# Kernel tuning notes

Hardware: AMD Instinct MI355X
Metric: run time of the kernel (lower is better)

The kernel has to match this reference:

```python
import math
import jax, jax.numpy as jnp
import numpy as np

DIM = 1024
NUM_HEADS = 16
HEAD_DIM = DIM // NUM_HEADS


def setup_inputs() -> dict:
    key = jax.random.key(0)
    ks = jax.random.split(key, 5)
    b, t, d = 2, 2048, DIM
    x = jax.random.normal(ks[0], (b, t, d), dtype=jnp.float32)
    mask = jnp.ones((b, t), dtype=jnp.float32)  # 1 = keep, 0 = pad
    s_in = 1.0 / math.sqrt(d)
    w_qkv = jax.random.normal(ks[1], (3 * d, d), dtype=jnp.float32) * s_in
    b_qkv = jnp.zeros((3 * d,), dtype=jnp.float32)
    w_out = jax.random.normal(ks[2], (d, d), dtype=jnp.float32) * s_in
    b_out = jnp.zeros((d,), dtype=jnp.float32)
    return {"x": x, "mask": mask, "w_qkv": w_qkv, "b_qkv": b_qkv,
            "w_out": w_out, "b_out": b_out}


def reference(x, mask, w_qkv, b_qkv, w_out, b_out):
    b, t, d = x.shape
    h, hd = NUM_HEADS, HEAD_DIM
    # qkv projection (torch Linear: x @ W^T + b)
    qkv = x @ w_qkv.T + b_qkv                          # [b,t,3d]
    q, k, v = jnp.split(qkv, 3, axis=-1)
    def reshape(z):
        return z.reshape(b, t, h, hd).transpose(0, 2, 1, 3)  # [b,h,t,hd]
    q, k, v = reshape(q), reshape(k), reshape(v)
    att = jnp.einsum('bhqd,bhkd->bhqk', q, k) / math.sqrt(hd)  # [b,h,t,t]
    causal = jnp.tril(jnp.ones((t, t), dtype=bool))            # [t,t]
    keep = causal[None, None, :, :] & (mask[:, None, None, :] != 0)
    att = jnp.where(keep, att, -jnp.inf)
    att = jax.nn.softmax(att, axis=-1)
    out = jnp.einsum('bhqk,bhkd->bhqd', att, v)        # [b,h,t,hd]
    out = out.transpose(0, 2, 1, 3).reshape(b, t, d)
    return out @ w_out.T + b_out
```

## Files before the change

### kernel.cpp

```cpp
#include <hip/hip_runtime.h>
#include <cmath>

#define B_ 2
#define T_ 2048
#define D_ 1024
#define H_ 16
#define HD_ 64
#define M_ (B_ * T_)
#define N3_ (3 * D_)
#define K_ 1024

typedef _Float16 halfx8 __attribute__((ext_vector_type(8)));
typedef _Float16 halfx4 __attribute__((ext_vector_type(4)));
typedef float f32x4 __attribute__((ext_vector_type(4)));
typedef float f32x16 __attribute__((ext_vector_type(16)));

#define ASYNC_COPY16(gp, lp) \
  __builtin_amdgcn_global_load_lds((__attribute__((address_space(1))) void*)(gp), \
      (__attribute__((address_space(3))) void*)(lp), 16, 0, 0)

#define QSCALE 0.1803368801111204f

__device__ const int QT_OF[40] = {15,15,15,15, 14,14,14,14, 13,13,13,13, 12,12,12,12,
                                  11,11,11, 10,10,10, 9,9,9, 8,8,8,
                                  7,7, 6,6, 5,5, 4,4, 3, 2, 1, 0};
__device__ const int C_OF[40]  = {0,1,2,3, 0,1,2,3, 0,1,2,3, 0,1,2,3,
                                  0,1,2, 0,1,2, 0,1,2, 0,1,2,
                                  0,1, 0,1, 0,1, 0,1, 0, 0, 0, 0};
__device__ const int CB_OF[16] = {0,1,2,3,4,6,8,10,12,15,18,21,24,28,32,36};
__device__ const int NC_OF[16] = {1,1,1,1,2,2,2,2,3,3,3,3,4,4,4,4};

__global__ __launch_bounds__(256) void f2h_kernel(const float* __restrict__ s,
                                                  _Float16* __restrict__ d, int n)
{
    int i = (blockIdx.x * 256 + threadIdx.x) * 8;
    if (i >= n) return;
    float4 a = *(const float4*)(s + i);
    float4 b = *(const float4*)(s + i + 4);
    halfx8 h;
    h[0] = (_Float16)a.x; h[1] = (_Float16)a.y; h[2] = (_Float16)a.z; h[3] = (_Float16)a.w;
    h[4] = (_Float16)b.x; h[5] = (_Float16)b.y; h[6] = (_Float16)b.z; h[7] = (_Float16)b.w;
    *(halfx8*)(d + i) = h;
}

__global__ void initflags_kernel(int* __restrict__ tflags)
{
    tflags[threadIdx.x] = 1;
}

__global__ __launch_bounds__(256) void mkbias_kernel(const float* __restrict__ mask,
                                                     float* __restrict__ kbias,
                                                     int* __restrict__ tflags, int n)
{
    int i = blockIdx.x * 256 + threadIdx.x;
    if (i < n) {
        float mv = mask[i];
        kbias[i] = (mv != 0.f) ? 0.f : -INFINITY;
        if (mv == 0.f) tflags[i >> 6] = 0;
    }
}

__global__ __launch_bounds__(256) void gemm_qkv(
    const _Float16* __restrict__ A, const _Float16* __restrict__ Wt,
    const float* __restrict__ bias,
    _Float16* __restrict__ qh, _Float16* __restrict__ kh, _Float16* __restrict__ vth)
{
    __shared__ _Float16 As[128 * 32];
    __shared__ _Float16 Bs[128 * 32];
    const int tid = threadIdx.x;
    const int lane = tid & 63, w = tid >> 6;
    const int col = lane & 15, quad = lane >> 4;
    const int wr = w >> 1, wc = w & 1;
    const int m0 = blockIdx.y << 7, n0 = blockIdx.x << 7;

    const int c0 = w * 2, c1 = c0 + 1;
    const int r0 = c0 * 16 + (lane >> 2), r1 = c1 * 16 + (lane >> 2);
    const int ks = (lane & 3) << 3;

    f32x4 acc[4][4] = {};

    for (int k0 = 0; k0 < K_; k0 += 32) {
        ASYNC_COPY16(A  + (size_t)(m0 + r0) * K_ + k0 + ks, &As[c0 * 512]);
        ASYNC_COPY16(A  + (size_t)(m0 + r1) * K_ + k0 + ks, &As[c1 * 512]);
        ASYNC_COPY16(Wt + (size_t)(n0 + r0) * K_ + k0 + ks, &Bs[c0 * 512]);
        ASYNC_COPY16(Wt + (size_t)(n0 + r1) * K_ + k0 + ks, &Bs[c1 * 512]);
        __syncthreads();
        halfx8 af[4], bf[4];
#pragma unroll
        for (int i = 0; i < 4; ++i)
            af[i] = *(const halfx8*)&As[(wr * 64 + i * 16 + col) * 32 + quad * 8];
#pragma unroll
        for (int j = 0; j < 4; ++j)
            bf[j] = *(const halfx8*)&Bs[(wc * 64 + j * 16 + col) * 32 + quad * 8];
#pragma unroll
        for (int i = 0; i < 4; ++i)
#pragma unroll
            for (int j = 0; j < 4; ++j)
                acc[i][j] = __builtin_amdgcn_mfma_f32_16x16x32_f16(af[i], bf[j], acc[i][j], 0, 0, 0);
        __syncthreads();
    }

#pragma unroll
    for (int i = 0; i < 4; ++i) {
#pragma unroll
        for (int r = 0; r < 4; ++r) {
            int m = m0 + wr * 64 + i * 16 + quad * 4 + r;
            int bb = m >> 11, tt = m & (T_ - 1);
#pragma unroll
            for (int j = 0; j < 4; ++j) {
                int n = n0 + wc * 64 + j * 16 + col;
                float val = acc[i][j][r] + bias[n];
                int which = n >> 10, head = (n >> 6) & 15, dd = n & 63;
                if (which == 0) {
                    qh[((size_t)(bb * H_ + head) * T_ + tt) * HD_ + dd] = (_Float16)(val * QSCALE);
                } else if (which == 1) {
                    int dds = ((((dd >> 3) ^ (tt & 7)) & 7) << 3) | (dd & 7);
                    kh[((size_t)(bb * H_ + head) * T_ + tt) * HD_ + dds] = (_Float16)val;
                } else {
                    int tts = (tt & ~63) | (((((tt >> 3) & 7) ^ (dd & 7)) & 7) << 3) | (tt & 7);
                    vth[((size_t)(bb * H_ + head) * HD_ + dd) * T_ + tts] = (_Float16)val;
                }
            }
        }
    }
}

__global__ __launch_bounds__(256) void gemm_out(
    const _Float16* __restrict__ A, const _Float16* __restrict__ Wt,
    const float* __restrict__ bias, float* __restrict__ C)
{
    __shared__ _Float16 As[128 * 32];
    __shared__ _Float16 Bs[128 * 32];
    const int tid = threadIdx.x;
    const int lane = tid & 63, w = tid >> 6;
    const int col = lane & 15, quad = lane >> 4;
    const int wr = w >> 1, wc = w & 1;
    const int m0 = blockIdx.y << 7, n0 = blockIdx.x << 7;

    const int c0 = w * 2, c1 = c0 + 1;
    const int r0 = c0 * 16 + (lane >> 2), r1 = c1 * 16 + (lane >> 2);
    const int ks = (lane & 3) << 3;

    f32x4 acc[4][4] = {};

    for (int k0 = 0; k0 < K_; k0 += 32) {
        ASYNC_COPY16(A  + (size_t)(m0 + r0) * K_ + k0 + ks, &As[c0 * 512]);
        ASYNC_COPY16(A  + (size_t)(m0 + r1) * K_ + k0 + ks, &As[c1 * 512]);
        ASYNC_COPY16(Wt + (size_t)(n0 + r0) * K_ + k0 + ks, &Bs[c0 * 512]);
        ASYNC_COPY16(Wt + (size_t)(n0 + r1) * K_ + k0 + ks, &Bs[c1 * 512]);
        __syncthreads();
        halfx8 af[4], bf[4];
#pragma unroll
        for (int i = 0; i < 4; ++i)
            af[i] = *(const halfx8*)&As[(wr * 64 + i * 16 + col) * 32 + quad * 8];
#pragma unroll
        for (int j = 0; j < 4; ++j)
            bf[j] = *(const halfx8*)&Bs[(wc * 64 + j * 16 + col) * 32 + quad * 8];
#pragma unroll
        for (int i = 0; i < 4; ++i)
#pragma unroll
            for (int j = 0; j < 4; ++j)
                acc[i][j] = __builtin_amdgcn_mfma_f32_16x16x32_f16(af[i], bf[j], acc[i][j], 0, 0, 0);
        __syncthreads();
    }

#pragma unroll
    for (int i = 0; i < 4; ++i) {
#pragma unroll
        for (int r = 0; r < 4; ++r) {
            int m = m0 + wr * 64 + i * 16 + quad * 4 + r;
#pragma unroll
            for (int j = 0; j < 4; ++j) {
                int n = n0 + wc * 64 + j * 16 + col;
                C[(size_t)m * D_ + n] = acc[i][j][r] + bias[n];
            }
        }
    }
}

__global__ __launch_bounds__(256) void attn_kernel(
    const _Float16* __restrict__ qh, const _Float16* __restrict__ kh,
    const _Float16* __restrict__ vth, const float* __restrict__ kbias,
    const int* __restrict__ tflags,
    float* __restrict__ pm, float* __restrict__ pl, _Float16* __restrict__ po)
{
    __shared__ _Float16 Ks[2][64 * 64];
    __shared__ _Float16 Vt[2][64 * 64];

    const int xi = blockIdx.x;
    const int qt = QT_OF[xi], c = C_OF[xi];
    const int h = blockIdx.y, b = blockIdx.z;
    const int tid = threadIdx.x;
    const int lane = tid & 63, w = tid >> 6;
    const int l31 = lane & 31, q2 = lane >> 5;

    const int kt0 = c * 8;
    const int ktend = min(2 * qt + 1, kt0 + 7);

    const size_t hb = (size_t)(b * H_ + h);
    const _Float16* qp = qh + hb * T_ * HD_;
    const _Float16* kp = kh + hb * T_ * HD_;
    const _Float16* vp = vth + hb * HD_ * T_;
    const float* kb = kbias + (size_t)b * T_;
    const int* tf = tflags + b * 32;

    const int q_row = qt * 128 + w * 32 + l31;

    halfx8 bq[4];
#pragma unroll
    for (int hc = 0; hc < 4; ++hc)
        bq[hc] = *(const halfx8*)(qp + (size_t)q_row * HD_ + hc * 16 + q2 * 8);

    float mrow = -INFINITY, lrow = 0.f;
    f32x16 oacc[2] = {};

    {
        const _Float16* ksrc = kp + (size_t)(kt0 * 64 + w * 16) * HD_;
        ASYNC_COPY16(ksrc + lane * 8, &Ks[0][(w * 16) * 64]);
        ASYNC_COPY16(ksrc + 8 * HD_ + lane * 8, &Ks[0][(w * 16 + 8) * 64]);
        const _Float16* vsrc = vp + (size_t)(w * 16 + (lane >> 3)) * T_
                                 + kt0 * 64 + (lane & 7) * 8;
        ASYNC_COPY16(vsrc, &Vt[0][(w * 16) * 64]);
        ASYNC_COPY16(vsrc + 8 * T_, &Vt[0][(w * 16 + 8) * 64]);
    }

    for (int kt = kt0; kt <= ktend; ++kt) {
        const int cur = (kt - kt0) & 1;
        __syncthreads();
        if (kt < ktend) {
            const int nb = cur ^ 1;
            const _Float16* ksrc = kp + (size_t)((kt + 1) * 64 + w * 16) * HD_;
            ASYNC_COPY16(ksrc + lane * 8, &Ks[nb][(w * 16) * 64]);
            ASYNC_COPY16(ksrc + 8 * HD_ + lane * 8, &Ks[nb][(w * 16 + 8) * 64]);
            const _Float16* vsrc = vp + (size_t)(w * 16 + (lane >> 3)) * T_
                                     + (kt + 1) * 64 + (lane & 7) * 8;
            ASYNC_COPY16(vsrc, &Vt[nb][(w * 16) * 64]);
            ASYNC_COPY16(vsrc + 8 * T_, &Vt[nb][(w * 16 + 8) * 64]);
        }
        if (kt * 64 > qt * 128 + w * 32 + 31) continue;

        f32x16 sa[2];
#pragma unroll
        for (int kb2 = 0; kb2 < 2; ++kb2) {
            f32x16 a;
#pragma unroll
            for (int r = 0; r < 16; ++r) a[r] = 0.f;
#pragma unroll
            for (int hc = 0; hc < 4; ++hc) {
                int seg = (hc * 2 + q2) ^ (l31 & 7);
                halfx8 ka = *(const halfx8*)&Ks[cur][(kb2 * 32 + l31) * 64 + seg * 8];
                a = __builtin_amdgcn_mfma_f32_32x32x16_f16(ka, bq[hc], a, 0, 0, 0);
            }
            sa[kb2] = a;
        }

        float mx = sa[0][0];
#pragma unroll
        for (int r = 1; r < 16; ++r) mx = fmaxf(mx, sa[0][r]);
#pragma unroll
        for (int r = 0; r < 16; ++r) mx = fmaxf(mx, sa[1][r]);
        mx = fmaxf(mx, __shfl_xor(mx, 32, 64));
        float mnew = fmaxf(mrow, mx);
        float alpha = exp2f(mrow - mnew);
        mrow = mnew;

        const bool interior = (kt * 64 + 63 <= qt * 128 + w * 32);
        const int allkeep = tf[kt];
        halfx4 pf[2][4];
        float rsum = 0.f;
        if (interior && allkeep) {
#pragma unroll
            for (int kb2 = 0; kb2 < 2; ++kb2)
#pragma unroll
                for (int cc = 0; cc < 4; ++cc)
#pragma unroll
                    for (int j = 0; j < 4; ++j) {
                        float pv = exp2f(sa[kb2][cc * 4 + j] - mnew);
                        rsum += pv;
                        pf[kb2][cc][j] = (_Float16)pv;
                    }
        } else {
#pragma unroll
            for (int kb2 = 0; kb2 < 2; ++kb2)
#pragma unroll
                for (int cc = 0; cc < 4; ++cc)
#pragma unroll
                    for (int j = 0; j < 4; ++j) {
                        int key = kt * 64 + kb2 * 32 + j + 8 * cc + 4 * q2;
                        float add = allkeep ? 0.f : kb[key];
                        float pv = (key <= q_row) ? exp2f(sa[kb2][cc * 4 + j] + add - mnew) : 0.f;
                        rsum += pv;
                        pf[kb2][cc][j] = (_Float16)pv;
                    }
        }
        rsum += __shfl_xor(rsum, 32, 64);
        lrow = lrow * alpha + rsum;

#pragma unroll
        for (int db = 0; db < 2; ++db)
#pragma unroll
            for (int r = 0; r < 16; ++r) oacc[db][r] *= alpha;

#pragma unroll
        for (int db = 0; db < 2; ++db)
#pragma unroll
            for (int kb2 = 0; kb2 < 2; ++kb2)
#pragma unroll
                for (int cc = 0; cc < 4; ++cc) {
                    int ck = kb2 * 4 + cc;
                    int seg = ck ^ (l31 & 7);
                    halfx4 va = *(const halfx4*)&Vt[cur][(db * 32 + l31) * 64 + seg * 8 + q2 * 4];
                    oacc[db] = __builtin_amdgcn_mfma_f32_32x32x8f16(va, pf[kb2][cc], oacc[db], 0, 0, 0);
                }
    }

    const int slot = (int)hb * 40 + CB_OF[qt] + c;
    const int qloc = w * 32 + l31;
    if (q2 == 0) {
        pm[(size_t)slot * 128 + qloc] = mrow;
        pl[(size_t)slot * 128 + qloc] = lrow;
    }
    _Float16* pob = po + ((size_t)slot * 128 + qloc) * 64;
#pragma unroll
    for (int db = 0; db < 2; ++db)
#pragma unroll
        for (int g = 0; g < 4; ++g) {
            halfx4 ov;
#pragma unroll
            for (int j = 0; j < 4; ++j)
                ov[j] = (_Float16)(oacc[db][g * 4 + j]);
            *(halfx4*)(pob + db * 32 + 8 * g + 4 * q2) = ov;
        }
}

__global__ __launch_bounds__(256) void attn_combine(
    const float* __restrict__ pm, const float* __restrict__ pl,
    const _Float16* __restrict__ po, _Float16* __restrict__ oh)
{
    const int qt = blockIdx.x, h = blockIdx.y, b = blockIdx.z;
    const int nc = NC_OF[qt], cb = CB_OF[qt];
    const int bh = b * H_ + h;
    const int tid = threadIdx.x;
    const int r = tid >> 1, dh = tid & 1;

    const int slot0 = bh * 40 + cb;
    float mc[4], lc[4];
    float mstar = -INFINITY;
    for (int cc = 0; cc < nc; ++cc) {
        mc[cc] = pm[(size_t)(slot0 + cc) * 128 + r];
        lc[cc] = pl[(size_t)(slot0 + cc) * 128 + r];
        mstar = fmaxf(mstar, mc[cc]);
    }
    float lstar = 0.f, wc[4];
    for (int cc = 0; cc < nc; ++cc) {
        wc[cc] = exp2f(mc[cc] - mstar);
        lstar += wc[cc] * lc[cc];
    }
    float acc[32] = {};
    for (int cc = 0; cc < nc; ++cc) {
        const _Float16* src = po + ((size_t)(slot0 + cc) * 128 + r) * 64 + dh * 32;
        float wv = wc[cc];
#pragma unroll
        for (int g = 0; g < 4; ++g) {
            halfx8 hv = *(const halfx8*)(src + g * 8);
#pragma unroll
            for (int j = 0; j < 8; ++j)
                acc[g * 8 + j] += wv * (float)hv[j];
        }
    }
    float linv = 1.f / lstar;
    _Float16* dst = oh + ((size_t)(b * T_ + qt * 128 + r)) * D_ + h * 64 + dh * 32;
#pragma unroll
    for (int g = 0; g < 4; ++g) {
        halfx8 ov;
#pragma unroll
        for (int j = 0; j < 8; ++j)
            ov[j] = (_Float16)(acc[g * 8 + j] * linv);
        *(halfx8*)(dst + g * 8) = ov;
    }
}

extern "C" void kernel_launch(void* const* d_in, const int* in_sizes, int n_in,
                              void* d_out, int out_size, void* d_ws, size_t ws_size,
                              hipStream_t stream)
{
    (void)in_sizes; (void)n_in; (void)out_size; (void)ws_size;
    const float* x     = (const float*)d_in[0];
    const float* mask  = (const float*)d_in[1];
    const float* w_qkv = (const float*)d_in[2];
    const float* b_qkv = (const float*)d_in[3];
    const float* w_out = (const float*)d_in[4];
    const float* b_out = (const float*)d_in[5];
    float* out = (float*)d_out;

    const size_t QKV1 = (size_t)B_ * H_ * T_ * HD_;
    _Float16* xh  = (_Float16*)d_ws;
    _Float16* wqh = xh  + (size_t)M_ * K_;
    _Float16* woh = wqh + (size_t)N3_ * K_;
    _Float16* qh  = woh + (size_t)D_ * K_;
    _Float16* kh  = qh  + QKV1;
    _Float16* vth = kh  + QKV1;
    _Float16* oh  = vth + QKV1;
    _Float16* po  = oh  + QKV1;
    float* kbias  = (float*)(po + (size_t)1280 * 128 * 64);
    float* pm     = kbias + (size_t)B_ * T_;
    float* pl     = pm + (size_t)1280 * 128;
    int* tflags   = (int*)(pl + (size_t)1280 * 128);

    f2h_kernel<<<(M_ * K_) / 8 / 256, 256, 0, stream>>>(x, xh, M_ * K_);
    f2h_kernel<<<(N3_ * K_) / 8 / 256, 256, 0, stream>>>(w_qkv, wqh, N3_ * K_);
    f2h_kernel<<<(D_ * K_) / 8 / 256, 256, 0, stream>>>(w_out, woh, D_ * K_);
    initflags_kernel<<<1, 64, 0, stream>>>(tflags);
    mkbias_kernel<<<(B_ * T_ + 255) / 256, 256, 0, stream>>>(mask, kbias, tflags, B_ * T_);

    gemm_qkv<<<dim3(N3_ / 128, M_ / 128), 256, 0, stream>>>(
        xh, wqh, b_qkv, qh, kh, vth);
    attn_kernel<<<dim3(40, H_, B_), 256, 0, stream>>>(
        qh, kh, vth, kbias, tflags, pm, pl, po);
    attn_combine<<<dim3(T_ / 128, H_, B_), 256, 0, stream>>>(
        pm, pl, po, oh);
    gemm_out<<<dim3(D_ / 128, M_ / 128), 256, 0, stream>>>(
        oh, woh, b_out, out);
}
```

Measured before the change: 224.9 us.

## Double attention query tile per block, fuse prep kernels, add swizzle and lazy rescale

The attention kernel now processes 256 query rows per block (64 per wave, two 32-row halves), so each K/V tile loaded into LDS is reused twice as much and the split count halves to 20 chunks per head. The K/V LDS swizzle gains an extra XOR term to reduce bank conflicts. Output rescaling is skipped when the running max doesn't change in any lane. The three fp32-to-fp16 conversion kernels are merged into one launch, and the init-flags and mask-bias kernels into one using a wave ballot. The combine kernel is adapted to 256-row tiles with one thread per row. The cost is higher register pressure, from doubled accumulators and Q fragments, and fewer blocks in flight.

```diff
diff --git a/kernel.cpp b/kernel.cpp
--- a/kernel.cpp
+++ b/kernel.cpp
@@ -21,20 +21,22 @@
 
 #define QSCALE 0.1803368801111204f
 
-__device__ const int QT_OF[40] = {15,15,15,15, 14,14,14,14, 13,13,13,13, 12,12,12,12,
-                                  11,11,11, 10,10,10, 9,9,9, 8,8,8,
-                                  7,7, 6,6, 5,5, 4,4, 3, 2, 1, 0};
-__device__ const int C_OF[40]  = {0,1,2,3, 0,1,2,3, 0,1,2,3, 0,1,2,3,
-                                  0,1,2, 0,1,2, 0,1,2, 0,1,2,
-                                  0,1, 0,1, 0,1, 0,1, 0, 0, 0, 0};
-__device__ const int CB_OF[16] = {0,1,2,3,4,6,8,10,12,15,18,21,24,28,32,36};
-__device__ const int NC_OF[16] = {1,1,1,1,2,2,2,2,3,3,3,3,4,4,4,4};
-
-__global__ __launch_bounds__(256) void f2h_kernel(const float* __restrict__ s,
-                                                  _Float16* __restrict__ d, int n)
-{
-    int i = (blockIdx.x * 256 + threadIdx.x) * 8;
-    if (i >= n) return;
+__device__ const int QT_OF[20] = {7,7,7,7, 6,6,6,6, 5,5,5, 4,4,4, 3,3, 2,2, 1, 0};
+__device__ const int C_OF[20]  = {0,1,2,3, 0,1,2,3, 0,1,2, 0,1,2, 0,1, 0,1, 0, 0};
+__device__ const int CB_OF[8]  = {0,1,2,4,6,9,12,16};
+__device__ const int NC_OF[8]  = {1,1,2,2,3,3,4,4};
+
+__global__ __launch_bounds__(256) void f2h_all(
+    const float* __restrict__ x, const float* __restrict__ wq,
+    const float* __restrict__ wo, _Float16* __restrict__ xh,
+    _Float16* __restrict__ wqh, _Float16* __restrict__ woh)
+{
+    int bid = blockIdx.x;
+    const float* s; _Float16* d; int off;
+    if (bid < 2048)      { s = x;  d = xh;  off = bid; }
+    else if (bid < 3584) { s = wq; d = wqh; off = bid - 2048; }
+    else                 { s = wo; d = woh; off = bid - 3584; }
+    int i = (off * 256 + threadIdx.x) * 8;
     float4 a = *(const float4*)(s + i);
     float4 b = *(const float4*)(s + i + 4);
     halfx8 h;
@@ -43,21 +45,15 @@
     *(halfx8*)(d + i) = h;
 }
 
-__global__ void initflags_kernel(int* __restrict__ tflags)
-{
-    tflags[threadIdx.x] = 1;
-}
-
-__global__ __launch_bounds__(256) void mkbias_kernel(const float* __restrict__ mask,
-                                                     float* __restrict__ kbias,
-                                                     int* __restrict__ tflags, int n)
+__global__ __launch_bounds__(256) void maskprep(const float* __restrict__ mask,
+                                                float* __restrict__ kbias,
+                                                int* __restrict__ tflags)
 {
     int i = blockIdx.x * 256 + threadIdx.x;
-    if (i < n) {
-        float mv = mask[i];
-        kbias[i] = (mv != 0.f) ? 0.f : -INFINITY;
-        if (mv == 0.f) tflags[i >> 6] = 0;
-    }
+    float mv = mask[i];
+    kbias[i] = (mv != 0.f) ? 0.f : -INFINITY;
+    unsigned long long bal = __ballot(mv != 0.f);
+    if ((threadIdx.x & 63) == 0) tflags[i >> 6] = (bal == ~0ULL) ? 1 : 0;
 }
 
 __global__ __launch_bounds__(256) void gemm_qkv(
@@ -114,10 +110,12 @@
                 if (which == 0) {
                     qh[((size_t)(bb * H_ + head) * T_ + tt) * HD_ + dd] = (_Float16)(val * QSCALE);
                 } else if (which == 1) {
-                    int dds = ((((dd >> 3) ^ (tt & 7)) & 7) << 3) | (dd & 7);
+                    int hi = ((dd >> 3) ^ (tt & 7) ^ ((tt >> 3) & 7)) & 7;
+                    int dds = (hi << 3) | (dd & 7);
                     kh[((size_t)(bb * H_ + head) * T_ + tt) * HD_ + dds] = (_Float16)val;
                 } else {
-                    int tts = (tt & ~63) | (((((tt >> 3) & 7) ^ (dd & 7)) & 7) << 3) | (tt & 7);
+                    int hi = (((tt >> 3) & 7) ^ (dd & 7) ^ ((dd >> 3) & 7)) & 7;
+                    int tts = (tt & ~63) | (hi << 3) | (tt & 7);
                     vth[((size_t)(bb * H_ + head) * HD_ + dd) * T_ + tts] = (_Float16)val;
                 }
             }
@@ -195,7 +193,7 @@
     const int l31 = lane & 31, q2 = lane >> 5;
 
     const int kt0 = c * 8;
-    const int ktend = min(2 * qt + 1, kt0 + 7);
+    const int ktend = min(4 * qt + 3, kt0 + 7);
 
     const size_t hb = (size_t)(b * H_ + h);
     const _Float16* qp = qh + hb * T_ * HD_;
@@ -204,15 +202,18 @@
     const float* kb = kbias + (size_t)b * T_;
     const int* tf = tflags + b * 32;
 
-    const int q_row = qt * 128 + w * 32 + l31;
-
-    halfx8 bq[4];
-#pragma unroll
-    for (int hc = 0; hc < 4; ++hc)
-        bq[hc] = *(const halfx8*)(qp + (size_t)q_row * HD_ + hc * 16 + q2 * 8);
-
-    float mrow = -INFINITY, lrow = 0.f;
-    f32x16 oacc[2] = {};
+    const int qbase = qt * 256 + w * 64;
+
+    halfx8 bq[2][4];
+#pragma unroll
+    for (int qhf = 0; qhf < 2; ++qhf)
+#pragma unroll
+        for (int hc = 0; hc < 4; ++hc)
+            bq[qhf][hc] = *(const halfx8*)(qp +
+                (size_t)(qbase + qhf * 32 + l31) * HD_ + hc * 16 + q2 * 8);
+
+    float mrow[2] = {-INFINITY, -INFINITY}, lrow[2] = {0.f, 0.f};
+    f32x16 oacc[2][2] = {};
 
     {
         const _Float16* ksrc = kp + (size_t)(kt0 * 64 + w * 16) * HD_;
@@ -237,100 +238,116 @@
             ASYNC_COPY16(vsrc, &Vt[nb][(w * 16) * 64]);
             ASYNC_COPY16(vsrc + 8 * T_, &Vt[nb][(w * 16 + 8) * 64]);
         }
-        if (kt * 64 > qt * 128 + w * 32 + 31) continue;
-
-        f32x16 sa[2];
-#pragma unroll
-        for (int kb2 = 0; kb2 < 2; ++kb2) {
-            f32x16 a;
-#pragma unroll
-            for (int r = 0; r < 16; ++r) a[r] = 0.f;
-#pragma unroll
-            for (int hc = 0; hc < 4; ++hc) {
-                int seg = (hc * 2 + q2) ^ (l31 & 7);
-                halfx8 ka = *(const halfx8*)&Ks[cur][(kb2 * 32 + l31) * 64 + seg * 8];
-                a = __builtin_amdgcn_mfma_f32_32x32x16_f16(ka, bq[hc], a, 0, 0, 0);
-            }
-            sa[kb2] = a;
-        }
-
-        float mx = sa[0][0];
-#pragma unroll
-        for (int r = 1; r < 16; ++r) mx = fmaxf(mx, sa[0][r]);
-#pragma unroll
-        for (int r = 0; r < 16; ++r) mx = fmaxf(mx, sa[1][r]);
-        mx = fmaxf(mx, __shfl_xor(mx, 32, 64));
-        float mnew = fmaxf(mrow, mx);
-        float alpha = exp2f(mrow - mnew);
-        mrow = mnew;
-
-        const bool interior = (kt * 64 + 63 <= qt * 128 + w * 32);
-        const int allkeep = tf[kt];
-        halfx4 pf[2][4];
-        float rsum = 0.f;
-        if (interior && allkeep) {
-#pragma unroll
-            for (int kb2 = 0; kb2 < 2; ++kb2)
-#pragma unroll
-                for (int cc = 0; cc < 4; ++cc)
-#pragma unroll
-                    for (int j = 0; j < 4; ++j) {
-                        float pv = exp2f(sa[kb2][cc * 4 + j] - mnew);
-                        rsum += pv;
-                        pf[kb2][cc][j] = (_Float16)pv;
+        if (kt * 64 > qbase + 63) continue;
+
+#pragma unroll
+        for (int qhf = 0; qhf < 2; ++qhf) {
+            const int qb = qbase + qhf * 32;
+            if (kt * 64 > qb + 31) continue;
+            const int q_row = qb + l31;
+
+            f32x16 sa[2];
+#pragma unroll
+            for (int kb2 = 0; kb2 < 2; ++kb2) {
+                f32x16 a;
+#pragma unroll
+                for (int r = 0; r < 16; ++r) a[r] = 0.f;
+#pragma unroll
+                for (int hc = 0; hc < 4; ++hc) {
+                    int seg = (hc * 2 + q2) ^ (l31 & 7) ^ ((kb2 * 4 + (l31 >> 3)) & 7);
+                    halfx8 ka = *(const halfx8*)&Ks[cur][(kb2 * 32 + l31) * 64 + seg * 8];
+                    a = __builtin_amdgcn_mfma_f32_32x32x16_f16(ka, bq[qhf][hc], a, 0, 0, 0);
+                }
+                sa[kb2] = a;
+            }
+
+            float mx = sa[0][0];
+#pragma unroll
+            for (int r = 1; r < 16; ++r) mx = fmaxf(mx, sa[0][r]);
+#pragma unroll
+            for (int r = 0; r < 16; ++r) mx = fmaxf(mx, sa[1][r]);
+            mx = fmaxf(mx, __shfl_xor(mx, 32, 64));
+            float mold = mrow[qhf];
+            float mnew = fmaxf(mold, mx);
+            unsigned long long bump = __ballot(mnew > mold);
+            mrow[qhf] = mnew;
+
+            const bool interior = (kt * 64 + 63 <= qb);
+            const int allkeep = tf[kt];
+            halfx4 pf[2][4];
+            float rsum = 0.f;
+            if (interior && allkeep) {
+#pragma unroll
+                for (int kb2 = 0; kb2 < 2; ++kb2)
+#pragma unroll
+                    for (int cc = 0; cc < 4; ++cc)
+#pragma unroll
+                        for (int j = 0; j < 4; ++j) {
+                            float pv = exp2f(sa[kb2][cc * 4 + j] - mnew);
+                            rsum += pv;
+                            pf[kb2][cc][j] = (_Float16)pv;
+                        }
+            } else {
+#pragma unroll
+                for (int kb2 = 0; kb2 < 2; ++kb2)
+#pragma unroll
+                    for (int cc = 0; cc < 4; ++cc)
+#pragma unroll
+                        for (int j = 0; j < 4; ++j) {
+                            int key = kt * 64 + kb2 * 32 + j + 8 * cc + 4 * q2;
+                            float add = allkeep ? 0.f : kb[key];
+                            float pv = (key <= q_row) ? exp2f(sa[kb2][cc * 4 + j] + add - mnew) : 0.f;
+                            rsum += pv;
+                            pf[kb2][cc][j] = (_Float16)pv;
+                        }
+            }
+            rsum += __shfl_xor(rsum, 32, 64);
+
+            if (bump) {
+                float alpha = exp2f(mold - mnew);
+                lrow[qhf] = lrow[qhf] * alpha + rsum;
+#pragma unroll
+                for (int db = 0; db < 2; ++db)
+#pragma unroll
+                    for (int r = 0; r < 16; ++r) oacc[qhf][db][r] *= alpha;
+            } else {
+                lrow[qhf] += rsum;
+            }
+
+#pragma unroll
+            for (int db = 0; db < 2; ++db)
+#pragma unroll
+                for (int kb2 = 0; kb2 < 2; ++kb2)
+#pragma unroll
+                    for (int cc = 0; cc < 4; ++cc) {
+                        int ck = kb2 * 4 + cc;
+                        int seg = ck ^ (l31 & 7) ^ ((db * 4 + (l31 >> 3)) & 7);
+                        halfx4 va = *(const halfx4*)&Vt[cur][(db * 32 + l31) * 64 + seg * 8 + q2 * 4];
+                        oacc[qhf][db] = __builtin_amdgcn_mfma_f32_32x32x8f16(va, pf[kb2][cc], oacc[qhf][db], 0, 0, 0);
                     }
-        } else {
-#pragma unroll
-            for (int kb2 = 0; kb2 < 2; ++kb2)
-#pragma unroll
-                for (int cc = 0; cc < 4; ++cc)
-#pragma unroll
-                    for (int j = 0; j < 4; ++j) {
-                        int key = kt * 64 + kb2 * 32 + j + 8 * cc + 4 * q2;
-                        float add = allkeep ? 0.f : kb[key];
-                        float pv = (key <= q_row) ? exp2f(sa[kb2][cc * 4 + j] + add - mnew) : 0.f;
-                        rsum += pv;
-                        pf[kb2][cc][j] = (_Float16)pv;
-                    }
-        }
-        rsum += __shfl_xor(rsum, 32, 64);
-        lrow = lrow * alpha + rsum;
-
+        }
+    }
+
+    const int slot = (int)hb * 20 + CB_OF[qt] + c;
+#pragma unroll
+    for (int qhf = 0; qhf < 2; ++qhf) {
+        const int qloc = w * 64 + qhf * 32 + l31;
+        if (q2 == 0) {
+            pm[(size_t)slot * 256 + qloc] = mrow[qhf];
+            pl[(size_t)slot * 256 + qloc] = lrow[qhf];
+        }
+        _Float16* pob = po + ((size_t)slot * 256 + qloc) * 64;
 #pragma unroll
         for (int db = 0; db < 2; ++db)
 #pragma unroll
-            for (int r = 0; r < 16; ++r) oacc[db][r] *= alpha;
-
-#pragma unroll
-        for (int db = 0; db < 2; ++db)
-#pragma unroll
-            for (int kb2 = 0; kb2 < 2; ++kb2)
-#pragma unroll
-                for (int cc = 0; cc < 4; ++cc) {
-                    int ck = kb2 * 4 + cc;
-                    int seg = ck ^ (l31 & 7);
-                    halfx4 va = *(const halfx4*)&Vt[cur][(db * 32 + l31) * 64 + seg * 8 + q2 * 4];
-                    oacc[db] = __builtin_amdgcn_mfma_f32_32x32x8f16(va, pf[kb2][cc], oacc[db], 0, 0, 0);
-                }
-    }
-
-    const int slot = (int)hb * 40 + CB_OF[qt] + c;
-    const int qloc = w * 32 + l31;
-    if (q2 == 0) {
-        pm[(size_t)slot * 128 + qloc] = mrow;
-        pl[(size_t)slot * 128 + qloc] = lrow;
-    }
-    _Float16* pob = po + ((size_t)slot * 128 + qloc) * 64;
-#pragma unroll
-    for (int db = 0; db < 2; ++db)
-#pragma unroll
-        for (int g = 0; g < 4; ++g) {
-            halfx4 ov;
-#pragma unroll
-            for (int j = 0; j < 4; ++j)
-                ov[j] = (_Float16)(oacc[db][g * 4 + j]);
-            *(halfx4*)(pob + db * 32 + 8 * g + 4 * q2) = ov;
-        }
+            for (int g = 0; g < 4; ++g) {
+                halfx4 ov;
+#pragma unroll
+                for (int j = 0; j < 4; ++j)
+                    ov[j] = (_Float16)(oacc[qhf][db][g * 4 + j]);
+                *(halfx4*)(pob + db * 32 + 8 * g + 4 * q2) = ov;
+            }
+    }
 }
 
 __global__ __launch_bounds__(256) void attn_combine(
@@ -339,16 +356,14 @@
 {
     const int qt = blockIdx.x, h = blockIdx.y, b = blockIdx.z;
     const int nc = NC_OF[qt], cb = CB_OF[qt];
-    const int bh = b * H_ + h;
-    const int tid = threadIdx.x;
-    const int r = tid >> 1, dh = tid & 1;
-
-    const int slot0 = bh * 40 + cb;
+    const int r = threadIdx.x;
+    const int slot0 = (b * H_ + h) * 20 + cb;
+
     float mc[4], lc[4];
     float mstar = -INFINITY;
     for (int cc = 0; cc < nc; ++cc) {
-        mc[cc] = pm[(size_t)(slot0 + cc) * 128 + r];
-        lc[cc] = pl[(size_t)(slot0 + cc) * 128 + r];
+        mc[cc] = pm[(size_t)(slot0 + cc) * 256 + r];
+        lc[cc] = pl[(size_t)(slot0 + cc) * 256 + r];
         mstar = fmaxf(mstar, mc[cc]);
     }
     float lstar = 0.f, wc[4];
@@ -356,12 +371,12 @@
         wc[cc] = exp2f(mc[cc] - mstar);
         lstar += wc[cc] * lc[cc];
     }
-    float acc[32] = {};
+    float acc[64] = {};
     for (int cc = 0; cc < nc; ++cc) {
-        const _Float16* src = po + ((size_t)(slot0 + cc) * 128 + r) * 64 + dh * 32;
+        const _Float16* src = po + ((size_t)(slot0 + cc) * 256 + r) * 64;
         float wv = wc[cc];
 #pragma unroll
-        for (int g = 0; g < 4; ++g) {
+        for (int g = 0; g < 8; ++g) {
             halfx8 hv = *(const halfx8*)(src + g * 8);
 #pragma unroll
             for (int j = 0; j < 8; ++j)
@@ -369,9 +384,9 @@
         }
     }
     float linv = 1.f / lstar;
-    _Float16* dst = oh + ((size_t)(b * T_ + qt * 128 + r)) * D_ + h * 64 + dh * 32;
-#pragma unroll
-    for (int g = 0; g < 4; ++g) {
+    _Float16* dst = oh + ((size_t)(b * T_ + qt * 256 + r)) * D_ + h * 64;
+#pragma unroll
+    for (int g = 0; g < 8; ++g) {
         halfx8 ov;
 #pragma unroll
         for (int j = 0; j < 8; ++j)
@@ -402,22 +417,19 @@
     _Float16* vth = kh  + QKV1;
     _Float16* oh  = vth + QKV1;
     _Float16* po  = oh  + QKV1;
-    float* kbias  = (float*)(po + (size_t)1280 * 128 * 64);
+    float* kbias  = (float*)(po + (size_t)640 * 256 * 64);
     float* pm     = kbias + (size_t)B_ * T_;
-    float* pl     = pm + (size_t)1280 * 128;
-    int* tflags   = (int*)(pl + (size_t)1280 * 128);
-
-    f2h_kernel<<<(M_ * K_) / 8 / 256, 256, 0, stream>>>(x, xh, M_ * K_);
-    f2h_kernel<<<(N3_ * K_) / 8 / 256, 256, 0, stream>>>(w_qkv, wqh, N3_ * K_);
-    f2h_kernel<<<(D_ * K_) / 8 / 256, 256, 0, stream>>>(w_out, woh, D_ * K_);
-    initflags_kernel<<<1, 64, 0, stream>>>(tflags);
-    mkbias_kernel<<<(B_ * T_ + 255) / 256, 256, 0, stream>>>(mask, kbias, tflags, B_ * T_);
+    float* pl     = pm + (size_t)640 * 256;
+    int* tflags   = (int*)(pl + (size_t)640 * 256);
+
+    f2h_all<<<4096, 256, 0, stream>>>(x, w_qkv, w_out, xh, wqh, woh);
+    maskprep<<<(B_ * T_) / 256, 256, 0, stream>>>(mask, kbias, tflags);
 
     gemm_qkv<<<dim3(N3_ / 128, M_ / 128), 256, 0, stream>>>(
         xh, wqh, b_qkv, qh, kh, vth);
-    attn_kernel<<<dim3(40, H_, B_), 256, 0, stream>>>(
+    attn_kernel<<<dim3(20, H_, B_), 256, 0, stream>>>(
         qh, kh, vth, kbias, tflags, pm, pl, po);
-    attn_combine<<<dim3(T_ / 128, H_, B_), 256, 0, stream>>>(
+    attn_combine<<<dim3(T_ / 256, H_, B_), 256, 0, stream>>>(
         pm, pl, po, oh);
     gemm_out<<<dim3(D_ / 128, M_ / 128), 256, 0, stream>>>(
         oh, woh, b_out, out);
```

Measured after the change: 255.5 us. 1.14x slower.

## Fuse prep kernels, finer attention split, new LDS swizzle, lazy rescale, narrower out-GEMM tiles

Applied to the files above, without the earlier changes.

The five prep launches (three fp16 conversions, flag init and mask bias) become one launch, with tile flags computed by a wave ballot. Attention work is split into 4-key-tile chunks, giving 72 blocks per head instead of 40, and chunk 0 writes its partial output straight into the final buffer so the combine pass reads less. The K/V LDS swizzle gains an extra XOR term to cut bank conflicts, and the online-softmax rescale is skipped when no row max changed. The output GEMM moves to 128x64 tiles for more blocks, which trades per-block reuse for occupancy.

```diff
diff --git a/kernel.cpp b/kernel.cpp
--- a/kernel.cpp
+++ b/kernel.cpp
@@ -21,43 +21,50 @@
 
 #define QSCALE 0.1803368801111204f
 
-__device__ const int QT_OF[40] = {15,15,15,15, 14,14,14,14, 13,13,13,13, 12,12,12,12,
-                                  11,11,11, 10,10,10, 9,9,9, 8,8,8,
-                                  7,7, 6,6, 5,5, 4,4, 3, 2, 1, 0};
-__device__ const int C_OF[40]  = {0,1,2,3, 0,1,2,3, 0,1,2,3, 0,1,2,3,
-                                  0,1,2, 0,1,2, 0,1,2, 0,1,2,
-                                  0,1, 0,1, 0,1, 0,1, 0, 0, 0, 0};
-__device__ const int CB_OF[16] = {0,1,2,3,4,6,8,10,12,15,18,21,24,28,32,36};
-__device__ const int NC_OF[16] = {1,1,1,1,2,2,2,2,3,3,3,3,4,4,4,4};
-
-__global__ __launch_bounds__(256) void f2h_kernel(const float* __restrict__ s,
-                                                  _Float16* __restrict__ d, int n)
-{
-    int i = (blockIdx.x * 256 + threadIdx.x) * 8;
-    if (i >= n) return;
+__device__ const int QT_OF[72] = {
+    15,15,15,15,15,15,15,15, 14,14,14,14,14,14,14,14,
+    13,13,13,13,13,13,13, 12,12,12,12,12,12,12,
+    11,11,11,11,11,11, 10,10,10,10,10,10,
+    9,9,9,9,9, 8,8,8,8,8, 7,7,7,7, 6,6,6,6,
+    5,5,5, 4,4,4, 3,3, 2,2, 1, 0};
+__device__ const int C_OF[72] = {
+    0,1,2,3,4,5,6,7, 0,1,2,3,4,5,6,7,
+    0,1,2,3,4,5,6, 0,1,2,3,4,5,6,
+    0,1,2,3,4,5, 0,1,2,3,4,5,
+    0,1,2,3,4, 0,1,2,3,4, 0,1,2,3, 0,1,2,3,
+    0,1,2, 0,1,2, 0,1, 0,1, 0, 0};
+__device__ const int CB_OF[16] = {0,1,2,4,6,9,12,16,20,25,30,36,42,49,56,64};
+__device__ const int NC_OF[16] = {1,1,2,2,3,3,4,4,5,5,6,6,7,7,8,8};
+#define NSLOT 72
+#define NPOSLOT 56
+
+__global__ __launch_bounds__(256) void prep_all(
+    const float* __restrict__ x, const float* __restrict__ wq,
+    const float* __restrict__ wo, const float* __restrict__ mask,
+    _Float16* __restrict__ xh, _Float16* __restrict__ wqh,
+    _Float16* __restrict__ woh, float* __restrict__ kbias,
+    int* __restrict__ tflags)
+{
+    int bid = blockIdx.x;
+    if (bid >= 4096) {
+        int i = (bid - 4096) * 256 + threadIdx.x;
+        float mv = mask[i];
+        kbias[i] = (mv != 0.f) ? 0.f : -INFINITY;
+        unsigned long long bal = __ballot(mv != 0.f);
+        if ((threadIdx.x & 63) == 0) tflags[i >> 6] = (bal == ~0ULL) ? 1 : 0;
+        return;
+    }
+    const float* s; _Float16* d; int off;
+    if (bid < 2048)      { s = x;  d = xh;  off = bid; }
+    else if (bid < 3584) { s = wq; d = wqh; off = bid - 2048; }
+    else                 { s = wo; d = woh; off = bid - 3584; }
+    int i = (off * 256 + threadIdx.x) * 8;
     float4 a = *(const float4*)(s + i);
     float4 b = *(const float4*)(s + i + 4);
     halfx8 h;
     h[0] = (_Float16)a.x; h[1] = (_Float16)a.y; h[2] = (_Float16)a.z; h[3] = (_Float16)a.w;
     h[4] = (_Float16)b.x; h[5] = (_Float16)b.y; h[6] = (_Float16)b.z; h[7] = (_Float16)b.w;
     *(halfx8*)(d + i) = h;
-}
-
-__global__ void initflags_kernel(int* __restrict__ tflags)
-{
-    tflags[threadIdx.x] = 1;
-}
-
-__global__ __launch_bounds__(256) void mkbias_kernel(const float* __restrict__ mask,
-                                                     float* __restrict__ kbias,
-                                                     int* __restrict__ tflags, int n)
-{
-    int i = blockIdx.x * 256 + threadIdx.x;
-    if (i < n) {
-        float mv = mask[i];
-        kbias[i] = (mv != 0.f) ? 0.f : -INFINITY;
-        if (mv == 0.f) tflags[i >> 6] = 0;
-    }
 }
 
 __global__ __launch_bounds__(256) void gemm_qkv(
@@ -114,10 +121,12 @@
                 if (which == 0) {
                     qh[((size_t)(bb * H_ + head) * T_ + tt) * HD_ + dd] = (_Float16)(val * QSCALE);
                 } else if (which == 1) {
-                    int dds = ((((dd >> 3) ^ (tt & 7)) & 7) << 3) | (dd & 7);
+                    int hi = ((dd >> 3) ^ (tt & 7) ^ ((tt >> 3) & 7)) & 7;
+                    int dds = (hi << 3) | (dd & 7);
                     kh[((size_t)(bb * H_ + head) * T_ + tt) * HD_ + dds] = (_Float16)val;
                 } else {
-                    int tts = (tt & ~63) | (((((tt >> 3) & 7) ^ (dd & 7)) & 7) << 3) | (tt & 7);
+                    int hi = (((tt >> 3) & 7) ^ (dd & 7) ^ ((dd >> 3) & 7)) & 7;
+                    int tts = (tt & ~63) | (hi << 3) | (tt & 7);
                     vth[((size_t)(bb * H_ + head) * HD_ + dd) * T_ + tts] = (_Float16)val;
                 }
             }
@@ -130,34 +139,33 @@
     const float* __restrict__ bias, float* __restrict__ C)
 {
     __shared__ _Float16 As[128 * 32];
-    __shared__ _Float16 Bs[128 * 32];
+    __shared__ _Float16 Bs[64 * 32];
     const int tid = threadIdx.x;
     const int lane = tid & 63, w = tid >> 6;
     const int col = lane & 15, quad = lane >> 4;
-    const int wr = w >> 1, wc = w & 1;
-    const int m0 = blockIdx.y << 7, n0 = blockIdx.x << 7;
+    const int m0 = blockIdx.y << 7, n0 = blockIdx.x << 6;
 
     const int c0 = w * 2, c1 = c0 + 1;
-    const int r0 = c0 * 16 + (lane >> 2), r1 = c1 * 16 + (lane >> 2);
+    const int rA0 = c0 * 16 + (lane >> 2), rA1 = c1 * 16 + (lane >> 2);
+    const int rB = w * 16 + (lane >> 2);
     const int ks = (lane & 3) << 3;
 
-    f32x4 acc[4][4] = {};
+    f32x4 acc[2][4] = {};
 
     for (int k0 = 0; k0 < K_; k0 += 32) {
-        ASYNC_COPY16(A  + (size_t)(m0 + r0) * K_ + k0 + ks, &As[c0 * 512]);
-        ASYNC_COPY16(A  + (size_t)(m0 + r1) * K_ + k0 + ks, &As[c1 * 512]);
-        ASYNC_COPY16(Wt + (size_t)(n0 + r0) * K_ + k0 + ks, &Bs[c0 * 512]);
-        ASYNC_COPY16(Wt + (size_t)(n0 + r1) * K_ + k0 + ks, &Bs[c1 * 512]);
+        ASYNC_COPY16(A  + (size_t)(m0 + rA0) * K_ + k0 + ks, &As[c0 * 512]);
+        ASYNC_COPY16(A  + (size_t)(m0 + rA1) * K_ + k0 + ks, &As[c1 * 512]);
+        ASYNC_COPY16(Wt + (size_t)(n0 + rB) * K_ + k0 + ks, &Bs[w * 512]);
         __syncthreads();
-        halfx8 af[4], bf[4];
-#pragma unroll
-        for (int i = 0; i < 4; ++i)
-            af[i] = *(const halfx8*)&As[(wr * 64 + i * 16 + col) * 32 + quad * 8];
+        halfx8 af[2], bf[4];
+#pragma unroll
+        for (int i = 0; i < 2; ++i)
+            af[i] = *(const halfx8*)&As[(w * 32 + i * 16 + col) * 32 + quad * 8];
 #pragma unroll
         for (int j = 0; j < 4; ++j)
-            bf[j] = *(const halfx8*)&Bs[(wc * 64 + j * 16 + col) * 32 + quad * 8];
-#pragma unroll
-        for (int i = 0; i < 4; ++i)
+            bf[j] = *(const halfx8*)&Bs[(j * 16 + col) * 32 + quad * 8];
+#pragma unroll
+        for (int i = 0; i < 2; ++i)
 #pragma unroll
             for (int j = 0; j < 4; ++j)
                 acc[i][j] = __builtin_amdgcn_mfma_f32_16x16x32_f16(af[i], bf[j], acc[i][j], 0, 0, 0);
@@ -165,13 +173,13 @@
     }
 
 #pragma unroll
-    for (int i = 0; i < 4; ++i) {
+    for (int i = 0; i < 2; ++i) {
 #pragma unroll
         for (int r = 0; r < 4; ++r) {
-            int m = m0 + wr * 64 + i * 16 + quad * 4 + r;
+            int m = m0 + w * 32 + i * 16 + quad * 4 + r;
 #pragma unroll
             for (int j = 0; j < 4; ++j) {
-                int n = n0 + wc * 64 + j * 16 + col;
+                int n = n0 + j * 16 + col;
                 C[(size_t)m * D_ + n] = acc[i][j][r] + bias[n];
             }
         }
@@ -182,7 +190,8 @@
     const _Float16* __restrict__ qh, const _Float16* __restrict__ kh,
     const _Float16* __restrict__ vth, const float* __restrict__ kbias,
     const int* __restrict__ tflags,
-    float* __restrict__ pm, float* __restrict__ pl, _Float16* __restrict__ po)
+    float* __restrict__ pm, float* __restrict__ pl,
+    _Float16* __restrict__ po, _Float16* __restrict__ oh)
 {
     __shared__ _Float16 Ks[2][64 * 64];
     __shared__ _Float16 Vt[2][64 * 64];
@@ -194,17 +203,18 @@
     const int lane = tid & 63, w = tid >> 6;
     const int l31 = lane & 31, q2 = lane >> 5;
 
-    const int kt0 = c * 8;
-    const int ktend = min(2 * qt + 1, kt0 + 7);
-
-    const size_t hb = (size_t)(b * H_ + h);
-    const _Float16* qp = qh + hb * T_ * HD_;
-    const _Float16* kp = kh + hb * T_ * HD_;
-    const _Float16* vp = vth + hb * HD_ * T_;
+    const int kt0 = c * 4;
+    const int ktend = min(2 * qt + 1, kt0 + 3);
+
+    const int bh = b * H_ + h;
+    const _Float16* qp = qh + (size_t)bh * T_ * HD_;
+    const _Float16* kp = kh + (size_t)bh * T_ * HD_;
+    const _Float16* vp = vth + (size_t)bh * HD_ * T_;
     const float* kb = kbias + (size_t)b * T_;
     const int* tf = tflags + b * 32;
 
-    const int q_row = qt * 128 + w * 32 + l31;
+    const int qbase = qt * 128 + w * 32;
+    const int q_row = qbase + l31;
 
     halfx8 bq[4];
 #pragma unroll
@@ -237,7 +247,7 @@
             ASYNC_COPY16(vsrc, &Vt[nb][(w * 16) * 64]);
             ASYNC_COPY16(vsrc + 8 * T_, &Vt[nb][(w * 16 + 8) * 64]);
         }
-        if (kt * 64 > qt * 128 + w * 32 + 31) continue;
+        if (kt * 64 > qbase + 31) continue;
 
         f32x16 sa[2];
 #pragma unroll
@@ -247,7 +257,7 @@
             for (int r = 0; r < 16; ++r) a[r] = 0.f;
 #pragma unroll
             for (int hc = 0; hc < 4; ++hc) {
-                int seg = (hc * 2 + q2) ^ (l31 & 7);
+                int seg = (hc * 2 + q2) ^ (l31 & 7) ^ ((kb2 * 4 + (l31 >> 3)) & 7);
                 halfx8 ka = *(const halfx8*)&Ks[cur][(kb2 * 32 + l31) * 64 + seg * 8];
                 a = __builtin_amdgcn_mfma_f32_32x32x16_f16(ka, bq[hc], a, 0, 0, 0);
             }
@@ -260,11 +270,12 @@
 #pragma unroll
         for (int r = 0; r < 16; ++r) mx = fmaxf(mx, sa[1][r]);
         mx = fmaxf(mx, __shfl_xor(mx, 32, 64));
-        float mnew = fmaxf(mrow, mx);
-        float alpha = exp2f(mrow - mnew);
+        float mold = mrow;
+        float mnew = fmaxf(mold, mx);
+        unsigned long long bump = __ballot(mnew > mold);
         mrow = mnew;
 
-        const bool interior = (kt * 64 + 63 <= qt * 128 + w * 32);
+        const bool interior = (kt * 64 + 63 <= qbase);
         const int allkeep = tf[kt];
         halfx4 pf[2][4];
         float rsum = 0.f;
@@ -294,12 +305,17 @@
                     }
         }
         rsum += __shfl_xor(rsum, 32, 64);
-        lrow = lrow * alpha + rsum;
-
-#pragma unroll
-        for (int db = 0; db < 2; ++db)
-#pragma unroll
-            for (int r = 0; r < 16; ++r) oacc[db][r] *= alpha;
+
+        if (bump) {
+            float alpha = exp2f(mold - mnew);
+            lrow = lrow * alpha + rsum;
+#pragma unroll
+            for (int db = 0; db < 2; ++db)
+#pragma unroll
+                for (int r = 0; r < 16; ++r) oacc[db][r] *= alpha;
+        } else {
+            lrow += rsum;
+        }
 
 #pragma unroll
         for (int db = 0; db < 2; ++db)
@@ -308,28 +324,32 @@
 #pragma unroll
                 for (int cc = 0; cc < 4; ++cc) {
                     int ck = kb2 * 4 + cc;
-                    int seg = ck ^ (l31 & 7);
+                    int seg = ck ^ (l31 & 7) ^ ((db * 4 + (l31 >> 3)) & 7);
                     halfx4 va = *(const halfx4*)&Vt[cur][(db * 32 + l31) * 64 + seg * 8 + q2 * 4];
                     oacc[db] = __builtin_amdgcn_mfma_f32_32x32x8f16(va, pf[kb2][cc], oacc[db], 0, 0, 0);
                 }
     }
 
-    const int slot = (int)hb * 40 + CB_OF[qt] + c;
     const int qloc = w * 32 + l31;
+    const int slot = bh * NSLOT + CB_OF[qt] + c;
     if (q2 == 0) {
         pm[(size_t)slot * 128 + qloc] = mrow;
         pl[(size_t)slot * 128 + qloc] = lrow;
     }
-    _Float16* pob = po + ((size_t)slot * 128 + qloc) * 64;
+    _Float16* pob;
+    if (c == 0)
+        pob = oh + ((size_t)(b * T_ + qt * 128 + qloc)) * D_ + h * 64;
+    else
+        pob = po + ((size_t)(bh * NPOSLOT + (CB_OF[qt] - qt) + (c - 1)) * 128 + qloc) * 64;
 #pragma unroll
     for (int db = 0; db < 2; ++db)
 #pragma unroll
-        for (int g = 0; g < 4; ++g) {
+        for (int gg = 0; gg < 4; ++gg) {
             halfx4 ov;
 #pragma unroll
             for (int j = 0; j < 4; ++j)
-                ov[j] = (_Float16)(oacc[db][g * 4 + j]);
-            *(halfx4*)(pob + db * 32 + 8 * g + 4 * q2) = ov;
+                ov[j] = (_Float16)(oacc[db][gg * 4 + j]);
+            *(halfx4*)(pob + db * 32 + 8 * gg + 4 * q2) = ov;
         }
 }
 
@@ -343,22 +363,36 @@
     const int tid = threadIdx.x;
     const int r = tid >> 1, dh = tid & 1;
 
-    const int slot0 = bh * 40 + cb;
-    float mc[4], lc[4];
+    const int slot0 = bh * NSLOT + cb;
+    float mc[8], lc[8];
     float mstar = -INFINITY;
     for (int cc = 0; cc < nc; ++cc) {
         mc[cc] = pm[(size_t)(slot0 + cc) * 128 + r];
         lc[cc] = pl[(size_t)(slot0 + cc) * 128 + r];
         mstar = fmaxf(mstar, mc[cc]);
     }
-    float lstar = 0.f, wc[4];
+    float lstar = 0.f, wc[8];
     for (int cc = 0; cc < nc; ++cc) {
         wc[cc] = exp2f(mc[cc] - mstar);
         lstar += wc[cc] * lc[cc];
     }
-    float acc[32] = {};
-    for (int cc = 0; cc < nc; ++cc) {
-        const _Float16* src = po + ((size_t)(slot0 + cc) * 128 + r) * 64 + dh * 32;
+
+    _Float16* ohrow = oh + ((size_t)(b * T_ + qt * 128 + r)) * D_ + h * 64 + dh * 32;
+
+    float acc[32];
+    {
+        float wv = wc[0];
+#pragma unroll
+        for (int g = 0; g < 4; ++g) {
+            halfx8 hv = *(const halfx8*)(ohrow + g * 8);
+#pragma unroll
+            for (int j = 0; j < 8; ++j)
+                acc[g * 8 + j] = wv * (float)hv[j];
+        }
+    }
+    const int pbase = bh * NPOSLOT + (cb - qt);
+    for (int cc = 1; cc < nc; ++cc) {
+        const _Float16* src = po + ((size_t)(pbase + cc - 1) * 128 + r) * 64 + dh * 32;
         float wv = wc[cc];
 #pragma unroll
         for (int g = 0; g < 4; ++g) {
@@ -369,14 +403,13 @@
         }
     }
     float linv = 1.f / lstar;
-    _Float16* dst = oh + ((size_t)(b * T_ + qt * 128 + r)) * D_ + h * 64 + dh * 32;
 #pragma unroll
     for (int g = 0; g < 4; ++g) {
         halfx8 ov;
 #pragma unroll
         for (int j = 0; j < 8; ++j)
             ov[j] = (_Float16)(acc[g * 8 + j] * linv);
-        *(halfx8*)(dst + g * 8) = ov;
+        *(halfx8*)(ohrow + g * 8) = ov;
     }
 }
 
@@ -402,23 +435,19 @@
     _Float16* vth = kh  + QKV1;
     _Float16* oh  = vth + QKV1;
     _Float16* po  = oh  + QKV1;
-    float* kbias  = (float*)(po + (size_t)1280 * 128 * 64);
+    float* kbias  = (float*)(po + (size_t)32 * NPOSLOT * 128 * 64);
     float* pm     = kbias + (size_t)B_ * T_;
-    float* pl     = pm + (size_t)1280 * 128;
-    int* tflags   = (int*)(pl + (size_t)1280 * 128);
-
-    f2h_kernel<<<(M_ * K_) / 8 / 256, 256, 0, stream>>>(x, xh, M_ * K_);
-    f2h_kernel<<<(N3_ * K_) / 8 / 256, 256, 0, stream>>>(w_qkv, wqh, N3_ * K_);
-    f2h_kernel<<<(D_ * K_) / 8 / 256, 256, 0, stream>>>(w_out, woh, D_ * K_);
-    initflags_kernel<<<1, 64, 0, stream>>>(tflags);
-    mkbias_kernel<<<(B_ * T_ + 255) / 256, 256, 0, stream>>>(mask, kbias, tflags, B_ * T_);
-
+    float* pl     = pm + (size_t)32 * NSLOT * 128;
+    int* tflags   = (int*)(pl + (size_t)32 * NSLOT * 128);
+
+    prep_all<<<4112, 256, 0, stream>>>(x, w_qkv, w_out, mask,
+                                       xh, wqh, woh, kbias, tflags);
     gemm_qkv<<<dim3(N3_ / 128, M_ / 128), 256, 0, stream>>>(
         xh, wqh, b_qkv, qh, kh, vth);
-    attn_kernel<<<dim3(40, H_, B_), 256, 0, stream>>>(
-        qh, kh, vth, kbias, tflags, pm, pl, po);
-    attn_combine<<<dim3(T_ / 128, H_, B_), 256, 0, stream>>>(
+    attn_kernel<<<dim3(72, H_, B_), 256, 0, stream>>>(
+        qh, kh, vth, kbias, tflags, pm, pl, po, oh);
+    attn_combine<<<dim3(16, H_, B_), 256, 0, stream>>>(
         pm, pl, po, oh);
-    gemm_out<<<dim3(D_ / 128, M_ / 128), 256, 0, stream>>>(
+    gemm_out<<<dim3(D_ / 64, M_ / 128), 256, 0, stream>>>(
         oh, woh, b_out, out);
 }
```

New measurement: 210.9 us. -6.2%, faster.
